# Kernel optimization log

Hardware: AMD Instinct MI355X
Metric: run time of the kernel (lower is better)

## Reference

```python
import jax, jax.numpy as jnp
import numpy as np

N = 100000; E = 1000000; D = 192; FD = 64; L = 6; MLP = 192
TW = 768; NPD = 6; CPD = 7; TEMP = 0.5; NREL = 2; EPS = 1e-5


def _ln(x, g, b):
    mu = jnp.mean(x, axis=-1, keepdims=True)
    var = jnp.mean(jnp.square(x - mu), axis=-1, keepdims=True)
    return (x - mu) * jax.lax.rsqrt(var + EPS) * g + b


def _bn(x, g, b):
    # BatchNorm1d in training mode: batch statistics over the N (node) axis
    mu = jnp.mean(x, axis=0, keepdims=True)
    var = jnp.mean(jnp.square(x - mu), axis=0, keepdims=True)
    return (x - mu) * jax.lax.rsqrt(var + EPS) * g + b


def _rgcn(x, Wrel, Wroot, bias, src, dst, etype):
    # PyG RGCNConv, aggr='mean': out_i = x_i @ Wroot + b + sum_r mean_{j in N_r(i)} x_j @ W_r
    out = x @ Wroot + bias
    for r in range(NREL):
        h = x @ Wrel[r]                                   # [N, D] per-relation transform
        mask = (etype == r)
        msg = jnp.where(mask[:, None], jnp.take(h, src, axis=0), 0.0)  # [E, D]
        agg = jax.ops.segment_sum(msg, dst, num_segments=N)
        cnt = jax.ops.segment_sum(mask.astype(x.dtype), dst, num_segments=N)
        out = out + agg / jnp.maximum(cnt, 1.0)[:, None]
    return out


def _forward(tweet, num_prop, comments_prop,
             Wt, bt, Wn, bnum, Wc, bc,
             Wv, bv, Wo, bo, ln1_g, ln1_b, bn_g, bn_b,
             W1, b1, W2, b2, ln2_g, ln2_b,
             Wrel, Wroot, rgcn_b, Wm1, bm1, Wm2, bm2, Wm3, bm3,
             edge_index, edge_type, labels, train_idx):
    lrelu = jax.nn.leaky_relu  # negative_slope=0.01, same as torch LeakyReLU default
    t = lrelu(tweet @ Wt + bt)
    n = lrelu(num_prop @ Wn + bnum)
    c = lrelu(comments_prop @ Wc + bc)
    x = jnp.concatenate([t, n, c], axis=1)  # [N, D]; seq dim of size 1 is elided
    for i in range(L):
        # MHA over seq_len=1: softmax over a single key is exactly 1, so
        # attn_out = out_proj(v_proj(x)); Q/K projections have zero effect/grad.
        v = x @ Wv[i] + bv[i]
        x = x + (v @ Wo[i] + bo[i])          # dropout in eval mode = identity
        x = _ln(x, ln1_g[i], ln1_b[i])
        x = _bn(x, bn_g[i], bn_b[i])
        f = lrelu(x @ W1[i] + b1[i]) @ W2[i] + b2[i]
        x = x + f
        x = _ln(x, ln2_g[i], ln2_b[i])
    # supervised contrastive loss on first train_idx nodes (train_idx static int)
    feat = x[:train_idx]
    lab = labels[:train_idx]
    fn = feat / jnp.linalg.norm(feat, axis=-1, keepdims=True)
    sim = (fn @ fn.T) / TEMP                              # [T, T]
    ex = jnp.exp(sim)
    match = (lab[:, None] == lab[None, :]).astype(x.dtype)
    closs = jnp.mean(-jnp.log(jnp.sum(match * ex, axis=1) / jnp.sum(ex, axis=1)))
    # two passes through the SAME (shared-weight) RGCN; dropout(p=0.1) eval = identity
    src, dst = edge_index[0], edge_index[1]
    h = _rgcn(x, Wrel, Wroot, rgcn_b, src, dst, edge_type)
    h = _rgcn(h, Wrel, Wroot, rgcn_b, src, dst, edge_type)
    h = lrelu(h @ Wm1 + bm1)
    h = lrelu(h @ Wm2 + bm2)
    logits = h @ Wm3 + bm3                                # [N, 2]
    return logits, closs


def setup_inputs() -> dict:
    key = jax.random.key(0)
    ks = iter(jax.random.split(key, 64))
    f32 = jnp.float32
    def p(*shape):
        fan_in = shape[-2] if len(shape) >= 2 else shape[-1]
        return jax.random.normal(next(ks), shape, f32) * (1.0 / np.sqrt(fan_in))
    inp = {
        'tweet': jax.random.normal(next(ks), (N, TW), f32),
        'num_prop': jax.random.normal(next(ks), (N, NPD), f32),
        'comments_prop': jax.random.normal(next(ks), (N, CPD), f32),
        'Wt': p(TW, FD), 'bt': jnp.zeros((FD,), f32),
        'Wn': p(NPD, FD), 'bnum': jnp.zeros((FD,), f32),
        'Wc': p(CPD, FD), 'bc': jnp.zeros((FD,), f32),
        'Wv': p(L, D, D), 'bv': jnp.zeros((L, D), f32),
        'Wo': p(L, D, D), 'bo': jnp.zeros((L, D), f32),
        'ln1_g': jnp.ones((L, D), f32), 'ln1_b': jnp.zeros((L, D), f32),
        'bn_g': jnp.ones((L, D), f32), 'bn_b': jnp.zeros((L, D), f32),
        'W1': p(L, D, MLP), 'b1': jnp.zeros((L, MLP), f32),
        'W2': p(L, MLP, D), 'b2': jnp.zeros((L, D), f32),
        'ln2_g': jnp.ones((L, D), f32), 'ln2_b': jnp.zeros((L, D), f32),
        'Wrel': p(NREL, D, D), 'Wroot': p(D, D), 'rgcn_b': jnp.zeros((D,), f32),
        'Wm1': p(D, MLP), 'bm1': jnp.zeros((MLP,), f32),
        'Wm2': p(MLP, D), 'bm2': jnp.zeros((D,), f32),
        'Wm3': p(D, 2), 'bm3': jnp.zeros((2,), f32),
        'edge_index': jax.random.randint(next(ks), (2, E), 0, N, jnp.int32),
        'edge_type': jax.random.randint(next(ks), (E,), 0, NREL, jnp.int32),
        'labels': jax.random.randint(next(ks), (N,), 0, 2, jnp.int32),
        'train_idx': 8192,
    }
    return inp


def reference(tweet, num_prop, comments_prop, Wt, bt, Wn, bnum, Wc, bc,
              Wv, bv, Wo, bo, ln1_g, ln1_b, bn_g, bn_b,
              W1, b1, W2, b2, ln2_g, ln2_b,
              Wrel, Wroot, rgcn_b, Wm1, bm1, Wm2, bm2, Wm3, bm3,
              edge_index, edge_type, labels, train_idx):
    return _forward(tweet, num_prop, comments_prop, Wt, bt, Wn, bnum, Wc, bc,
                    Wv, bv, Wo, bo, ln1_g, ln1_b, bn_g, bn_b,
                    W1, b1, W2, b2, ln2_g, ln2_b,
                    Wrel, Wroot, rgcn_b, Wm1, bm1, Wm2, bm2, Wm3, bm3,
                    edge_index, edge_type, labels, train_idx)
```

## Files before the change

kernel.cpp:

```cpp
#include <hip/hip_runtime.h>

#define NN 100000
#define EE 1000000
#define DDIM 192
#define NLAYER 6
#define TRAIN 8192
#define SLOPE 0.01f
#define EPS_LN 1e-5f
#define TOTSEG (2 * NN)
#define SCAN_NB 98

typedef float f32x4 __attribute__((ext_vector_type(4)));
typedef __bf16 bf16x8 __attribute__((ext_vector_type(8)));
typedef unsigned short ushort_t;
typedef unsigned int uint_t;

__device__ __forceinline__ float lrelu(float v) { return v > 0.0f ? v : SLOPE * v; }

__device__ __forceinline__ ushort_t f2bf(float f) {
    __bf16 h = (__bf16)f;
    return __builtin_bit_cast(ushort_t, h);
}

__device__ __forceinline__ float bf2f(ushort_t b) {
    union { uint_t u; float f; } v; v.u = ((uint_t)b) << 16; return v.f;
}

__device__ __forceinline__ float wave_sum(float s) {
    #pragma unroll
    for (int off = 32; off > 0; off >>= 1) s += __shfl_down(s, off);
    return __shfl(s, 0);
}

__global__ __launch_bounds__(256) void prep_w(
    const float* __restrict__ Wt, const float* __restrict__ Wv,
    const float* __restrict__ Wo, const float* __restrict__ W1,
    const float* __restrict__ W2, const float* __restrict__ Wrel,
    const float* __restrict__ Wroot, const float* __restrict__ Wm1,
    const float* __restrict__ Wm2, ushort_t* __restrict__ WTt,
    ushort_t* __restrict__ WTs, ushort_t* __restrict__ WTg)
{
    const int bid = blockIdx.x;
    if (bid < 29 * 144) {
        const int mat = bid / 144;
        const int o = (bid % 144) * 256 + threadIdx.x;
        const float* src;
        if      (mat <  6) src = Wv   + (size_t)mat * 36864;
        else if (mat < 12) src = Wo   + (size_t)(mat - 6)  * 36864;
        else if (mat < 18) src = W1   + (size_t)(mat - 12) * 36864;
        else if (mat < 24) src = W2   + (size_t)(mat - 18) * 36864;
        else if (mat < 26) src = Wrel + (size_t)(mat - 24) * 36864;
        else if (mat == 26) src = Wroot;
        else if (mat == 27) src = Wm1;
        else                src = Wm2;
        const int m = o / 192, k = o - m * 192;
        const ushort_t b = f2bf(src[(size_t)k * 192 + m]);
        if (mat == 24 || mat == 25)
            WTg[(size_t)m * 576 + 192 + (mat - 24) * 192 + k] = b;
        else if (mat == 26)
            WTg[(size_t)m * 576 + k] = b;
        else
            WTs[(size_t)mat * 36864 + o] = b;
    } else {
        const int o = (bid - 29 * 144) * 256 + threadIdx.x;
        const int m = o / 768, k = o - m * 768;
        WTt[o] = f2bf(Wt[(size_t)k * 64 + m]);
    }
}

__global__ __launch_bounds__(512) void gemm_tweet(
    const float* __restrict__ A, const ushort_t* __restrict__ WT,
    const float* __restrict__ bias, ushort_t* __restrict__ Cbf, int n)
{
    __shared__ ushort_t Ws[2][64 * 32];
    const int tid = threadIdx.x;
    const int lane = tid & 63, w = tid >> 6;
    const int quad = lane >> 4, l15 = lane & 15;
    const int row0 = blockIdx.x * 128;
    const int myrow = row0 + w * 16 + l15;
    const bool rok = myrow < n;

    f32x4 acc[4];
    #pragma unroll
    for (int nf = 0; nf < 4; ++nf) acc[nf] = (f32x4){0.f, 0.f, 0.f, 0.f};

    const float* aF = A + (size_t)myrow * 768 + quad * 8;

    auto stageW = [&](int t, int b) {
        if (tid < 256) {
            const int col = tid >> 2, part = tid & 3;
            *(uint4*)&Ws[b][col * 32 + part * 8] =
                *(const uint4*)(WT + (size_t)col * 768 + (t << 5) + part * 8);
        }
    };
    auto loadA = [&](int t, float* fo) {
        if (rok) {
            const float4 p0 = *(const float4*)(aF + t * 32);
            const float4 p1 = *(const float4*)(aF + t * 32 + 4);
            fo[0] = p0.x; fo[1] = p0.y; fo[2] = p0.z; fo[3] = p0.w;
            fo[4] = p1.x; fo[5] = p1.y; fo[6] = p1.z; fo[7] = p1.w;
        } else {
            #pragma unroll
            for (int i = 0; i < 8; ++i) fo[i] = 0.f;
        }
    };

    float fc[8];
    stageW(0, 0);
    loadA(0, fc);
    __syncthreads();
    #pragma unroll 2
    for (int t = 0; t < 24; ++t) {
        const int b = t & 1;
        if (t < 23) stageW(t + 1, b ^ 1);
        float fn[8];
        if (t < 23) loadA(t + 1, fn);
        union { uint_t u[4]; bf16x8 v; } r;
        #pragma unroll
        for (int i = 0; i < 4; ++i)
            r.u[i] = (uint_t)f2bf(fc[2 * i]) | ((uint_t)f2bf(fc[2 * i + 1]) << 16);
        #pragma unroll
        for (int nf = 0; nf < 4; ++nf) {
            const bf16x8 bb = *(const bf16x8*)&Ws[b][(nf * 16 + l15) * 32 + quad * 8];
            acc[nf] = __builtin_amdgcn_mfma_f32_16x16x32_bf16(r.v, bb, acc[nf], 0, 0, 0);
        }
        __syncthreads();
        if (t < 23) {
            #pragma unroll
            for (int i = 0; i < 8; ++i) fc[i] = fn[i];
        }
    }

    #pragma unroll
    for (int reg = 0; reg < 4; ++reg) {
        const int gr = row0 + w * 16 + quad * 4 + reg;
        if (gr >= n) continue;
        #pragma unroll
        for (int nf = 0; nf < 4; ++nf) {
            const int col = nf * 16 + l15;
            Cbf[(size_t)gr * DDIM + col] = f2bf(lrelu(acc[nf][reg] + bias[col]));
        }
    }
}

template <bool RELU1, bool RELU2, bool RES, bool LNORM, bool BN,
          bool BNSTAT, bool CBF, bool LOGITS, bool FNORM>
__global__ __launch_bounds__(512, 4) void gemm2_mfma(
    const ushort_t* __restrict__ Ain, const ushort_t* __restrict__ wta,
    const float* __restrict__ bias1, const ushort_t* __restrict__ wtb,
    const float* __restrict__ bias2, const ushort_t* __restrict__ resin,
    ushort_t* __restrict__ Cbf,
    const float* __restrict__ bnsum, const float* __restrict__ bng,
    const float* __restrict__ bnb, float* __restrict__ bnacc,
    const float* __restrict__ lg, const float* __restrict__ lb,
    const float* __restrict__ Wm3, const float* __restrict__ bm3,
    float* __restrict__ outp, ushort_t* __restrict__ fnb, int n)
{
    constexpr int VST = 200;
    __shared__ ushort_t Vs[128 * VST];
    __shared__ ushort_t Ws[2][192 * 32];
    __shared__ float scs[DDIM], shs[DDIM];
    const int tid = threadIdx.x;
    const int lane = tid & 63, w = tid >> 6;
    const int quad = lane >> 4, l15 = lane & 15;
    const int row0 = blockIdx.x * 128;
    const int myrow = row0 + w * 16 + l15;
    const bool rok = myrow < n;

    if constexpr (BN) {
        const float invN = 1.0f / (float)NN;
        for (int j = tid; j < DDIM; j += 512) {
            const float mu = bnsum[j] * invN;
            const float var = bnsum[DDIM + j] * invN - mu * mu;
            const float sc = bng[j] * rsqrtf(var + EPS_LN);
            scs[j] = sc;
            shs[j] = fmaf(-mu, sc, bnb[j]);
        }
    }

    f32x4 acc[12];
    #pragma unroll
    for (int nf = 0; nf < 12; ++nf) acc[nf] = (f32x4){0.f, 0.f, 0.f, 0.f};

    const ushort_t* aB = Ain + (size_t)myrow * DDIM + quad * 8;

    auto stageW = [&](const ushort_t* wt, int t, int b) {
        const int k0 = t << 5;
        for (int s = tid; s < 768; s += 512) {
            const int col = s >> 2, part = s & 3;
            *(uint4*)&Ws[b][col * 32 + part * 8] =
                *(const uint4*)(wt + (size_t)col * DDIM + k0 + part * 8);
        }
    };
    auto loadA = [&](int t) -> uint4 {
        return rok ? *(const uint4*)(aB + t * 32) : make_uint4(0u, 0u, 0u, 0u);
    };
    auto makeA = [&](const uint4& ui, int t) -> bf16x8 {
        if constexpr (BN) {
            const int c0 = (t << 5) + quad * 8;
            const float4 sc0 = *(const float4*)&scs[c0];
            const float4 sc1 = *(const float4*)&scs[c0 + 4];
            const float4 sh0 = *(const float4*)&shs[c0];
            const float4 sh1 = *(const float4*)&shs[c0 + 4];
            const uint_t* uw = (const uint_t*)&ui;
            float x[8];
            #pragma unroll
            for (int i = 0; i < 4; ++i) {
                x[2 * i]     = bf2f((ushort_t)(uw[i] & 0xffffu));
                x[2 * i + 1] = bf2f((ushort_t)(uw[i] >> 16));
            }
            x[0] = fmaf(x[0], sc0.x, sh0.x); x[1] = fmaf(x[1], sc0.y, sh0.y);
            x[2] = fmaf(x[2], sc0.z, sh0.z); x[3] = fmaf(x[3], sc0.w, sh0.w);
            x[4] = fmaf(x[4], sc1.x, sh1.x); x[5] = fmaf(x[5], sc1.y, sh1.y);
            x[6] = fmaf(x[6], sc1.z, sh1.z); x[7] = fmaf(x[7], sc1.w, sh1.w);
            union { uint_t u[4]; bf16x8 v; } r;
            #pragma unroll
            for (int i = 0; i < 4; ++i)
                r.u[i] = (uint_t)f2bf(x[2 * i]) | ((uint_t)f2bf(x[2 * i + 1]) << 16);
            return r.v;
        } else {
            return __builtin_bit_cast(bf16x8, ui);
        }
    };

    uint4 uc;
    stageW(wta, 0, 0);
    uc = loadA(0);
    __syncthreads();
    #pragma unroll 2
    for (int t = 0; t < 6; ++t) {
        const int b = t & 1;
        if (t < 5) stageW(wta, t + 1, b ^ 1);
        uint4 un;
        if (t < 5) un = loadA(t + 1);
        const bf16x8 a = makeA(uc, t);
        #pragma unroll
        for (int nf = 0; nf < 12; ++nf) {
            const bf16x8 bb = *(const bf16x8*)&Ws[b][(nf * 16 + l15) * 32 + quad * 8];
            acc[nf] = __builtin_amdgcn_mfma_f32_16x16x32_bf16(a, bb, acc[nf], 0, 0, 0);
        }
        __syncthreads();
        if (t < 5) uc = un;
    }

    {
        float b1r[12];
        #pragma unroll
        for (int nf = 0; nf < 12; ++nf) b1r[nf] = bias1[nf * 16 + l15];
        #pragma unroll
        for (int reg = 0; reg < 4; ++reg) {
            ushort_t* vrow = &Vs[(w * 16 + quad * 4 + reg) * VST + l15];
            #pragma unroll
            for (int nf = 0; nf < 12; ++nf) {
                float x = acc[nf][reg] + b1r[nf];
                if (RELU1) x = lrelu(x);
                vrow[nf * 16] = f2bf(x);
                acc[nf][reg] = 0.f;
            }
        }
    }
    stageW(wtb, 0, 0);
    __syncthreads();

    #pragma unroll 2
    for (int t = 0; t < 6; ++t) {
        const int b = t & 1;
        if (t < 5) stageW(wtb, t + 1, b ^ 1);
        const bf16x8 a = *(const bf16x8*)&Vs[(w * 16 + l15) * VST + (t << 5) + quad * 8];
        #pragma unroll
        for (int nf = 0; nf < 12; ++nf) {
            const bf16x8 bb = *(const bf16x8*)&Ws[b][(nf * 16 + l15) * 32 + quad * 8];
            acc[nf] = __builtin_amdgcn_mfma_f32_16x16x32_bf16(a, bb, acc[nf], 0, 0, 0);
        }
        __syncthreads();
    }

    int   col[12];
    float bia[12];
    #pragma unroll
    for (int nf = 0; nf < 12; ++nf) {
        col[nf] = nf * 16 + l15;
        bia[nf] = bias2[col[nf]];
    }
    float rsc[12], rsh[12];
    if constexpr (BN && RES) {
        #pragma unroll
        for (int nf = 0; nf < 12; ++nf) {
            rsc[nf] = scs[col[nf]];
            rsh[nf] = shs[col[nf]];
        }
    }
    float w3a[12], w3b[12];
    if constexpr (LOGITS) {
        #pragma unroll
        for (int nf = 0; nf < 12; ++nf) {
            w3a[nf] = Wm3[col[nf] * 2 + 0];
            w3b[nf] = Wm3[col[nf] * 2 + 1];
        }
    }
    float cs[12], cs2[12];
    if constexpr (BNSTAT) {
        #pragma unroll
        for (int nf = 0; nf < 12; ++nf) { cs[nf] = 0.f; cs2[nf] = 0.f; }
    }
    #pragma unroll
    for (int reg = 0; reg < 4; ++reg) {
        const int gr = row0 + w * 16 + quad * 4 + reg;
        const bool ok = gr < n;
        float v[12];
        #pragma unroll
        for (int nf = 0; nf < 12; ++nf) {
            float x = acc[nf][reg] + bia[nf];
            if constexpr (RES) {
                float r = ok ? bf2f(resin[(size_t)gr * DDIM + col[nf]]) : 0.f;
                if constexpr (BN) r = fmaf(r, rsc[nf], rsh[nf]);
                x += r;
            }
            v[nf] = x;
        }
        if constexpr (LNORM) {
            float s = 0.f, s2 = 0.f;
            #pragma unroll
            for (int nf = 0; nf < 12; ++nf) { s += v[nf]; s2 = fmaf(v[nf], v[nf], s2); }
            #pragma unroll
            for (int off = 1; off < 16; off <<= 1) {
                s  += __shfl_xor(s, off);
                s2 += __shfl_xor(s2, off);
            }
            const float mu = s * (1.0f / DDIM);
            const float var = s2 * (1.0f / DDIM) - mu * mu;
            const float rs = rsqrtf(var + EPS_LN);
            #pragma unroll
            for (int nf = 0; nf < 12; ++nf)
                v[nf] = fmaf((v[nf] - mu) * rs, lg[col[nf]], lb[col[nf]]);
        }
        float s0 = 0.f, s1 = 0.f;
        #pragma unroll
        for (int nf = 0; nf < 12; ++nf) {
            float x = v[nf];
            if (RELU2) x = lrelu(x);
            if constexpr (BNSTAT) {
                const float xa = ok ? x : 0.f;
                cs[nf] += xa;
                cs2[nf] = fmaf(xa, xa, cs2[nf]);
            }
            if constexpr (LOGITS) {
                s0 = fmaf(x, w3a[nf], s0);
                s1 = fmaf(x, w3b[nf], s1);
            }
            if (ok) {
                if constexpr (CBF) Cbf[(size_t)gr * DDIM + col[nf]] = f2bf(x);
            }
        }
        if constexpr (LOGITS) {
            #pragma unroll
            for (int off = 1; off < 16; off <<= 1) {
                s0 += __shfl_xor(s0, off);
                s1 += __shfl_xor(s1, off);
            }
            if (l15 == 0 && ok) {
                outp[(size_t)gr * 2 + 0] = s0 + bm3[0];
                outp[(size_t)gr * 2 + 1] = s1 + bm3[1];
            }
        }
        if constexpr (FNORM) {
            if (gr < TRAIN) {
                float q = 0.f;
                #pragma unroll
                for (int nf = 0; nf < 12; ++nf) q = fmaf(v[nf], v[nf], q);
                #pragma unroll
                for (int off = 1; off < 16; off <<= 1) q += __shfl_xor(q, off);
                const float inv = 1.0f / sqrtf(q);
                #pragma unroll
                for (int nf = 0; nf < 12; ++nf)
                    fnb[(size_t)gr * DDIM + col[nf]] = f2bf(v[nf] * inv);
            }
        }
    }
    if constexpr (BNSTAT) {
        float* bsA = (float*)&Ws[0][0];
        float* bsB = bsA + 8 * 192;
        #pragma unroll
        for (int nf = 0; nf < 12; ++nf) {
            cs[nf]  += __shfl_xor(cs[nf], 16);  cs[nf]  += __shfl_xor(cs[nf], 32);
            cs2[nf] += __shfl_xor(cs2[nf], 16); cs2[nf] += __shfl_xor(cs2[nf], 32);
        }
        if (quad == 0) {
            #pragma unroll
            for (int nf = 0; nf < 12; ++nf) {
                bsA[w * 192 + col[nf]] = cs[nf];
                bsB[w * 192 + col[nf]] = cs2[nf];
            }
        }
        __syncthreads();
        if (tid < DDIM) {
            float s = 0.f, s2 = 0.f;
            #pragma unroll
            for (int k = 0; k < 8; ++k) {
                s  += bsA[k * 192 + tid];
                s2 += bsB[k * 192 + tid];
            }
            atomicAdd(&bnacc[tid], s);
            atomicAdd(&bnacc[DDIM + tid], s2);
        }
    }
}

__global__ __launch_bounds__(512, 4) void gemm_cat(
    const ushort_t* __restrict__ A1, const ushort_t* __restrict__ A2,
    const ushort_t* __restrict__ WT, const float* __restrict__ bias,
    ushort_t* __restrict__ Cbf, int n)
{
    __shared__ ushort_t Ws[2][192 * 32];
    const int tid = threadIdx.x;
    const int lane = tid & 63, w = tid >> 6;
    const int quad = lane >> 4, l15 = lane & 15;
    const int row0 = blockIdx.x * 128;
    const int myrow = row0 + w * 16 + l15;
    const bool rok = myrow < n;

    f32x4 acc[12];
    #pragma unroll
    for (int nf = 0; nf < 12; ++nf) acc[nf] = (f32x4){0.f, 0.f, 0.f, 0.f};

    const ushort_t* a1p = A1 + (size_t)myrow * 192 + quad * 8;
    const ushort_t* a2p = A2 + (size_t)myrow * 384 + quad * 8;

    auto stageW = [&](int t, int b) {
        const int k0 = t << 5;
        for (int s = tid; s < 768; s += 512) {
            const int col = s >> 2, part = s & 3;
            *(uint4*)&Ws[b][col * 32 + part * 8] =
                *(const uint4*)(WT + (size_t)col * 576 + k0 + part * 8);
        }
    };
    auto loadA = [&](int t) -> uint4 {
        if (!rok) return make_uint4(0u, 0u, 0u, 0u);
        const ushort_t* p = (t < 6) ? (a1p + t * 32) : (a2p + (t - 6) * 32);
        return *(const uint4*)p;
    };

    uint4 uc;
    stageW(0, 0);
    uc = loadA(0);
    __syncthreads();

    #pragma unroll 2
    for (int t = 0; t < 18; ++t) {
        const int b = t & 1;
        if (t < 17) stageW(t + 1, b ^ 1);
        uint4 un;
        if (t < 17) un = loadA(t + 1);
        const bf16x8 a = __builtin_bit_cast(bf16x8, uc);
        #pragma unroll
        for (int nf = 0; nf < 12; ++nf) {
            const bf16x8 bb = *(const bf16x8*)&Ws[b][(nf * 16 + l15) * 32 + quad * 8];
            acc[nf] = __builtin_amdgcn_mfma_f32_16x16x32_bf16(a, bb, acc[nf], 0, 0, 0);
        }
        __syncthreads();
        if (t < 17) uc = un;
    }

    #pragma unroll
    for (int reg = 0; reg < 4; ++reg) {
        const int gr = row0 + w * 16 + quad * 4 + reg;
        if (gr >= n) continue;
        #pragma unroll
        for (int nf = 0; nf < 12; ++nf) {
            const int col = nf * 16 + l15;
            Cbf[(size_t)gr * DDIM + col] = f2bf(acc[nf][reg] + bias[col]);
        }
    }
}

__global__ __launch_bounds__(256) void embed_nc_k(
    const float* __restrict__ np_, const float* __restrict__ cp,
    const float* __restrict__ Wn, const float* __restrict__ bnum,
    const float* __restrict__ Wc, const float* __restrict__ bc,
    ushort_t* __restrict__ xb)
{
    const int idx = blockIdx.x * 256 + threadIdx.x;
    if (idx >= NN * 128) return;
    const int node = idx >> 7;
    const int c = idx & 127;
    float acc;
    if (c < 64) {
        acc = bnum[c];
        #pragma unroll
        for (int k = 0; k < 6; ++k) acc = fmaf(np_[node * 6 + k], Wn[k * 64 + c], acc);
    } else {
        const int cc = c - 64;
        acc = bc[cc];
        #pragma unroll
        for (int k = 0; k < 7; ++k) acc = fmaf(cp[node * 7 + k], Wc[k * 64 + cc], acc);
    }
    xb[(size_t)node * DDIM + 64 + c] = f2bf(lrelu(acc));
}

__global__ __launch_bounds__(256) void sim_mfma(const ushort_t* __restrict__ fnb,
    const int* __restrict__ lab, float* __restrict__ row_ex, float* __restrict__ row_mt)
{
    __shared__ ushort_t Ai[128 * 32];
    __shared__ ushort_t Bj[128 * 32];
    __shared__ int Li[128], Lj[128];
    const int bid = blockIdx.x;
    int ti = (int)((sqrtf(8.0f * (float)bid + 1.0f) - 1.0f) * 0.5f);
    while ((ti + 1) * (ti + 2) / 2 <= bid) ++ti;
    while (ti * (ti + 1) / 2 > bid) --ti;
    const int tj = bid - ti * (ti + 1) / 2;
    const int i0 = ti * 128, j0 = tj * 128;
    const bool offd = (ti != tj);

    const int tid = threadIdx.x, lane = tid & 63, w = tid >> 6;
    const int quad = lane >> 4, l15 = lane & 15;
    if (tid < 128) Li[tid] = lab[i0 + tid];
    else           Lj[tid - 128] = lab[j0 + tid - 128];
    const int iw = (w >> 1) * 64, jw = (w & 1) * 64;

    f32x4 acc[4][4];
    #pragma unroll
    for (int m = 0; m < 4; ++m)
        #pragma unroll
        for (int nf = 0; nf < 4; ++nf)
            acc[m][nf] = (f32x4){0.f, 0.f, 0.f, 0.f};

    for (int k0 = 0; k0 < DDIM; k0 += 32) {
        #pragma unroll
        for (int s = tid; s < 512; s += 256) {
            const int row = s >> 2, part = s & 3;
            *(uint4*)&Ai[row * 32 + part * 8] =
                *(const uint4*)(fnb + (size_t)(i0 + row) * DDIM + k0 + part * 8);
            *(uint4*)&Bj[row * 32 + part * 8] =
                *(const uint4*)(fnb + (size_t)(j0 + row) * DDIM + k0 + part * 8);
        }
        __syncthreads();
        bf16x8 a[4], b[4];
        #pragma unroll
        for (int m = 0; m < 4; ++m)
            a[m] = *(const bf16x8*)&Ai[(iw + m * 16 + l15) * 32 + quad * 8];
        #pragma unroll
        for (int nf = 0; nf < 4; ++nf)
            b[nf] = *(const bf16x8*)&Bj[(jw + nf * 16 + l15) * 32 + quad * 8];
        #pragma unroll
        for (int m = 0; m < 4; ++m)
            #pragma unroll
            for (int nf = 0; nf < 4; ++nf)
                acc[m][nf] = __builtin_amdgcn_mfma_f32_16x16x32_bf16(a[m], b[nf], acc[m][nf], 0, 0, 0);
        __syncthreads();
    }

    int lj[4];
    #pragma unroll
    for (int nf = 0; nf < 4; ++nf) lj[nf] = Lj[jw + nf * 16 + l15];
    float ce[4], cm[4];
    #pragma unroll
    for (int nf = 0; nf < 4; ++nf) { ce[nf] = 0.f; cm[nf] = 0.f; }

    #pragma unroll
    for (int m = 0; m < 4; ++m) {
        #pragma unroll
        for (int reg = 0; reg < 4; ++reg) {
            const int rl = iw + m * 16 + quad * 4 + reg;
            const int li = Li[rl];
            float se = 0.f, sm = 0.f;
            #pragma unroll
            for (int nf = 0; nf < 4; ++nf) {
                const float e = __expf(acc[m][nf][reg] * 2.0f);
                se += e;
                const bool mt = (li == lj[nf]);
                if (mt) sm += e;
                if (offd) {
                    ce[nf] += e;
                    if (mt) cm[nf] += e;
                }
            }
            #pragma unroll
            for (int off = 1; off < 16; off <<= 1) {
                se += __shfl_xor(se, off);
                sm += __shfl_xor(sm, off);
            }
            if (l15 == 0) {
                atomicAdd(&row_ex[i0 + rl], se);
                atomicAdd(&row_mt[i0 + rl], sm);
            }
        }
    }
    if (offd) {
        #pragma unroll
        for (int nf = 0; nf < 4; ++nf) {
            ce[nf] += __shfl_xor(ce[nf], 16); ce[nf] += __shfl_xor(ce[nf], 32);
            cm[nf] += __shfl_xor(cm[nf], 16); cm[nf] += __shfl_xor(cm[nf], 32);
        }
        if (quad == 0) {
            #pragma unroll
            for (int nf = 0; nf < 4; ++nf) {
                atomicAdd(&row_ex[j0 + jw + nf * 16 + l15], ce[nf]);
                atomicAdd(&row_mt[j0 + jw + nf * 16 + l15], cm[nf]);
            }
        }
    }
}

__global__ __launch_bounds__(256) void closs_k(const float* __restrict__ ex,
    const float* __restrict__ mt, float* __restrict__ out)
{
    float s = 0.f;
    for (int i = threadIdx.x; i < TRAIN; i += 256) s += -logf(mt[i] / ex[i]);
    s = wave_sum(s);
    __shared__ float red[4];
    const int wave = threadIdx.x >> 6, lane = threadIdx.x & 63;
    if (lane == 0) red[wave] = s;
    __syncthreads();
    if (threadIdx.x == 0) out[0] = (red[0] + red[1] + red[2] + red[3]) / (float)TRAIN;
}

__global__ __launch_bounds__(256) void cnt_i_k(const int* __restrict__ dst,
    const int* __restrict__ ety, int* __restrict__ cnti)
{
    const int e = blockIdx.x * 256 + threadIdx.x;
    if (e >= EE) return;
    atomicAdd(&cnti[(size_t)ety[e] * NN + dst[e]], 1);
}

__global__ __launch_bounds__(256) void part_k(const int* __restrict__ cnti,
                                              int* __restrict__ part)
{
    __shared__ int sh[256];
    const int tid = threadIdx.x;
    const int i0 = blockIdx.x * 2048 + tid * 8;
    int s = 0;
    #pragma unroll
    for (int j = 0; j < 8; ++j) {
        const int i = i0 + j;
        s += (i < TOTSEG) ? cnti[i] : 0;
    }
    sh[tid] = s;
    __syncthreads();
    #pragma unroll
    for (int off = 128; off > 0; off >>= 1) {
        if (tid < off) sh[tid] += sh[tid + off];
        __syncthreads();
    }
    if (tid == 0) part[blockIdx.x] = sh[0];
}

__global__ __launch_bounds__(128) void scanp_k(int* __restrict__ part)
{
    __shared__ int sh[128];
    const int tid = threadIdx.x;
    const int v = (tid < SCAN_NB) ? part[tid] : 0;
    sh[tid] = v;
    __syncthreads();
    #pragma unroll
    for (int off = 1; off < 128; off <<= 1) {
        const int t = (tid >= off) ? sh[tid - off] : 0;
        __syncthreads();
        sh[tid] += t;
        __syncthreads();
    }
    if (tid < SCAN_NB) part[tid] = sh[tid] - v;
}

__global__ __launch_bounds__(256) void offs_k(const int* __restrict__ cnti,
    const int* __restrict__ part, int* __restrict__ offs)
{
    __shared__ int sh[256];
    const int tid = threadIdx.x;
    const int i0 = blockIdx.x * 2048 + tid * 8;
    int v[8];
    int loc = 0;
    #pragma unroll
    for (int j = 0; j < 8; ++j) {
        const int i = i0 + j;
        v[j] = (i < TOTSEG) ? cnti[i] : 0;
        loc += v[j];
    }
    sh[tid] = loc;
    __syncthreads();
    #pragma unroll
    for (int off = 1; off < 256; off <<= 1) {
        const int t = (tid >= off) ? sh[tid - off] : 0;
        __syncthreads();
        sh[tid] += t;
        __syncthreads();
    }
    int pre = part[blockIdx.x] + sh[tid] - loc;
    #pragma unroll
    for (int j = 0; j < 8; ++j) {
        const int i = i0 + j;
        if (i < TOTSEG) offs[i] = pre;
        pre += v[j];
    }
}

__global__ __launch_bounds__(256) void fill_k(const int* __restrict__ src,
    const int* __restrict__ dst, const int* __restrict__ ety,
    int* __restrict__ offs, int* __restrict__ elist)
{
    const int e = blockIdx.x * 256 + threadIdx.x;
    if (e >= EE) return;
    const int pos = atomicAdd(&offs[(size_t)ety[e] * NN + dst[e]], 1);
    elist[pos] = src[e];
}

__global__ __launch_bounds__(256) void gather_bf_k(const ushort_t* __restrict__ xb,
    const int* __restrict__ elist, const int* __restrict__ offs,
    const int* __restrict__ cnti, ushort_t* __restrict__ aggb)
{
    const int wave = threadIdx.x >> 6, lane = threadIdx.x & 63;
    const int d = blockIdx.x * 4 + wave;
    if (d >= NN) return;
    const bool lo = lane < 32;
    #pragma unroll
    for (int r = 0; r < 2; ++r) {
        const int seg = r * NN + d;
        const int end = offs[seg];
        const int c = cnti[seg];
        float a0 = 0.f, a1 = 0.f, b0 = 0.f, b1 = 0.f;
        int e = end - c;
        for (; e + 1 < end; e += 2) {
            const int s0 = elist[e], s1 = elist[e + 1];
            const uint_t* r0 = (const uint_t*)(xb + (size_t)s0 * DDIM);
            const uint_t* r1 = (const uint_t*)(xb + (size_t)s1 * DDIM);
            const uint_t x0 = r0[lane], x1 = r1[lane];
            uint_t y0 = 0u, y1 = 0u;
            if (lo) { y0 = r0[64 + lane]; y1 = r1[64 + lane]; }
            a0 += bf2f((ushort_t)(x0 & 0xffffu)) + bf2f((ushort_t)(x1 & 0xffffu));
            a1 += bf2f((ushort_t)(x0 >> 16))     + bf2f((ushort_t)(x1 >> 16));
            b0 += bf2f((ushort_t)(y0 & 0xffffu)) + bf2f((ushort_t)(y1 & 0xffffu));
            b1 += bf2f((ushort_t)(y0 >> 16))     + bf2f((ushort_t)(y1 >> 16));
        }
        if (e < end) {
            const int s0 = elist[e];
            const uint_t* r0 = (const uint_t*)(xb + (size_t)s0 * DDIM);
            const uint_t x0 = r0[lane];
            uint_t y0 = 0u;
            if (lo) y0 = r0[64 + lane];
            a0 += bf2f((ushort_t)(x0 & 0xffffu));
            a1 += bf2f((ushort_t)(x0 >> 16));
            b0 += bf2f((ushort_t)(y0 & 0xffffu));
            b1 += bf2f((ushort_t)(y0 >> 16));
        }
        const float inv = 1.0f / (float)max(c, 1);
        uint_t* ar = (uint_t*)(aggb + (size_t)d * 384 + r * DDIM);
        ar[lane] = (uint_t)f2bf(a0 * inv) | ((uint_t)f2bf(a1 * inv) << 16);
        if (lo)
            ar[64 + lane] = (uint_t)f2bf(b0 * inv) | ((uint_t)f2bf(b1 * inv) << 16);
    }
}

extern "C" void kernel_launch(void* const* d_in, const int* in_sizes, int n_in,
                              void* d_out, int out_size, void* d_ws, size_t ws_size,
                              hipStream_t stream)
{
    const float* tweet   = (const float*)d_in[0];
    const float* np_     = (const float*)d_in[1];
    const float* cp      = (const float*)d_in[2];
    const float* Wt      = (const float*)d_in[3];
    const float* bt      = (const float*)d_in[4];
    const float* Wn      = (const float*)d_in[5];
    const float* bnum    = (const float*)d_in[6];
    const float* Wc      = (const float*)d_in[7];
    const float* bc      = (const float*)d_in[8];
    const float* Wv      = (const float*)d_in[9];
    const float* bv      = (const float*)d_in[10];
    const float* Wo      = (const float*)d_in[11];
    const float* bo      = (const float*)d_in[12];
    const float* ln1g    = (const float*)d_in[13];
    const float* ln1b    = (const float*)d_in[14];
    const float* bng     = (const float*)d_in[15];
    const float* bnb     = (const float*)d_in[16];
    const float* W1      = (const float*)d_in[17];
    const float* b1      = (const float*)d_in[18];
    const float* W2      = (const float*)d_in[19];
    const float* b2      = (const float*)d_in[20];
    const float* ln2g    = (const float*)d_in[21];
    const float* ln2b    = (const float*)d_in[22];
    const float* Wrel    = (const float*)d_in[23];
    const float* Wroot   = (const float*)d_in[24];
    const float* rgcnb   = (const float*)d_in[25];
    const float* Wm1     = (const float*)d_in[26];
    const float* bm1     = (const float*)d_in[27];
    const float* Wm2     = (const float*)d_in[28];
    const float* bm2     = (const float*)d_in[29];
    const float* Wm3     = (const float*)d_in[30];
    const float* bm3     = (const float*)d_in[31];
    const int*   eidx    = (const int*)d_in[32];
    const int*   esrc    = eidx;
    const int*   edst    = eidx + EE;
    const int*   ety     = (const int*)d_in[33];
    const int*   labels  = (const int*)d_in[34];
    float* out = (float*)d_out;

    const size_t ND = (size_t)NN * DDIM;
    ushort_t* XBF  = (ushort_t*)d_ws;
    ushort_t* X1BF = XBF + ND;
    ushort_t* AGGB = X1BF + ND;
    ushort_t* FNb  = AGGB + 2 * ND;
    ushort_t* WTt  = FNb + (size_t)TRAIN * DDIM;
    ushort_t* WTs  = WTt + 49152;
    ushort_t* WTg  = WTs + (size_t)29 * 36864;
    float* ROWEX = (float*)(WTg + 110592);
    float* ROWMT = ROWEX + TRAIN;
    float* BNS   = ROWMT + TRAIN;
    int*   CNTI  = (int*)(BNS + 12 * DDIM);
    int*   OFFS  = CNTI + 2 * NN;
    int*   ELIST = OFFS + 2 * NN;
    int*   PART  = ELIST + EE;
    ushort_t* WTv  = WTs;
    ushort_t* WTo  = WTs + (size_t)6  * 36864;
    ushort_t* WT1  = WTs + (size_t)12 * 36864;
    ushort_t* WT2  = WTs + (size_t)18 * 36864;
    ushort_t* WTm1 = WTs + (size_t)27 * 36864;
    ushort_t* WTm2 = WTs + (size_t)28 * 36864;

    const int gx = (NN + 127) / 128;
    const dim3 blk(256);
    const dim3 blk5(512);

    prep_w<<<29 * 144 + 192, blk, 0, stream>>>(Wt, Wv, Wo, W1, W2, Wrel, Wroot, Wm1, Wm2, WTt, WTs, WTg);

    hipMemsetAsync(CNTI, 0, 2 * NN * sizeof(int), stream);
    cnt_i_k<<<(EE + 255) / 256, blk, 0, stream>>>(edst, ety, CNTI);
    part_k<<<SCAN_NB, blk, 0, stream>>>(CNTI, PART);
    scanp_k<<<1, 128, 0, stream>>>(PART);
    offs_k<<<SCAN_NB, blk, 0, stream>>>(CNTI, PART, OFFS);
    fill_k<<<(EE + 255) / 256, blk, 0, stream>>>(esrc, edst, ety, OFFS, ELIST);

    gemm_tweet<<<gx, blk5, 0, stream>>>(tweet, WTt, bt, XBF, NN);
    embed_nc_k<<<(NN * 128 + 255) / 256, blk, 0, stream>>>(np_, cp, Wn, bnum, Wc, bc, XBF);

    hipMemsetAsync(BNS, 0, 12 * DDIM * sizeof(float), stream);
    for (int i = 0; i < NLAYER; ++i) {
        const size_t wo = (size_t)i * 36864;
        float* bnacc_i = BNS + (size_t)i * 2 * DDIM;
        gemm2_mfma<false, false, true, true, false, true, true, false, false>
            <<<gx, blk5, 0, stream>>>(
            XBF, WTv + wo, bv + i * DDIM, WTo + wo, bo + i * DDIM, XBF,
            X1BF, nullptr, nullptr, nullptr, bnacc_i,
            ln1g + i * DDIM, ln1b + i * DDIM, nullptr, nullptr, nullptr, nullptr, NN);
        if (i < NLAYER - 1)
            gemm2_mfma<true, false, true, true, true, false, true, false, false>
                <<<gx, blk5, 0, stream>>>(
                X1BF, WT1 + wo, b1 + i * DDIM, WT2 + wo, b2 + i * DDIM, X1BF,
                XBF, bnacc_i, bng + i * DDIM, bnb + i * DDIM, nullptr,
                ln2g + i * DDIM, ln2b + i * DDIM, nullptr, nullptr, nullptr, nullptr, NN);
        else
            gemm2_mfma<true, false, true, true, true, false, true, false, true>
                <<<gx, blk5, 0, stream>>>(
                X1BF, WT1 + wo, b1 + i * DDIM, WT2 + wo, b2 + i * DDIM, X1BF,
                XBF, bnacc_i, bng + i * DDIM, bnb + i * DDIM, nullptr,
                ln2g + i * DDIM, ln2b + i * DDIM, nullptr, nullptr, nullptr, FNb, NN);
    }

    hipMemsetAsync(ROWEX, 0, 2 * TRAIN * sizeof(float), stream);
    sim_mfma<<<(TRAIN / 128) * (TRAIN / 128 + 1) / 2, blk, 0, stream>>>(FNb, labels, ROWEX, ROWMT);
    closs_k<<<1, blk, 0, stream>>>(ROWEX, ROWMT, out + 2 * (size_t)NN);

    gather_bf_k<<<(NN + 3) / 4, blk, 0, stream>>>(XBF, ELIST, OFFS, CNTI, AGGB);
    gemm_cat<<<gx, blk5, 0, stream>>>(XBF, AGGB, WTg, rgcnb, XBF, NN);

    gather_bf_k<<<(NN + 3) / 4, blk, 0, stream>>>(XBF, ELIST, OFFS, CNTI, AGGB);
    gemm_cat<<<gx, blk5, 0, stream>>>(XBF, AGGB, WTg, rgcnb, XBF, NN);

    gemm2_mfma<true, true, false, false, false, false, false, true, false>
        <<<gx, blk5, 0, stream>>>(
        XBF, WTm1, bm1, WTm2, bm2, nullptr, nullptr,
        nullptr, nullptr, nullptr, nullptr, nullptr, nullptr,
        Wm3, bm3, out, nullptr, NN);
}
```

Before: 1.852 ms.

## Stage GEMM epilogue outputs through LDS, fuse embeddings, split gather per relation

```diff
diff --git a/kernel.cpp b/kernel.cpp
--- a/kernel.cpp
+++ b/kernel.cpp
@@ -70,9 +70,15 @@
 
 __global__ __launch_bounds__(512) void gemm_tweet(
     const float* __restrict__ A, const ushort_t* __restrict__ WT,
-    const float* __restrict__ bias, ushort_t* __restrict__ Cbf, int n)
-{
+    const float* __restrict__ bias,
+    const float* __restrict__ np_, const float* __restrict__ cp,
+    const float* __restrict__ Wn, const float* __restrict__ bnum,
+    const float* __restrict__ Wc, const float* __restrict__ bc,
+    ushort_t* __restrict__ Cbf, int n)
+{
+    constexpr int VST = 200;
     __shared__ ushort_t Ws[2][64 * 32];
+    __shared__ ushort_t Cs[128 * VST];
     const int tid = threadIdx.x;
     const int lane = tid & 63, w = tid >> 6;
     const int quad = lane >> 4, l15 = lane & 15;
@@ -133,13 +139,38 @@
 
     #pragma unroll
     for (int reg = 0; reg < 4; ++reg) {
-        const int gr = row0 + w * 16 + quad * 4 + reg;
-        if (gr >= n) continue;
+        const int lrow = w * 16 + quad * 4 + reg;
+        const int gr = row0 + lrow;
         #pragma unroll
         for (int nf = 0; nf < 4; ++nf) {
             const int col = nf * 16 + l15;
-            Cbf[(size_t)gr * DDIM + col] = f2bf(lrelu(acc[nf][reg] + bias[col]));
-        }
+            Cs[lrow * VST + col] = f2bf(lrelu(acc[nf][reg] + bias[col]));
+        }
+        if (gr < n) {
+            const float* nrow = np_ + (size_t)gr * 6;
+            const float* crow = cp + (size_t)gr * 7;
+            for (int cj = 64 + l15; cj < 192; cj += 16) {
+                float a;
+                if (cj < 128) {
+                    const int c = cj - 64;
+                    a = bnum[c];
+                    #pragma unroll
+                    for (int k = 0; k < 6; ++k) a = fmaf(nrow[k], Wn[k * 64 + c], a);
+                } else {
+                    const int cc = cj - 128;
+                    a = bc[cc];
+                    #pragma unroll
+                    for (int k = 0; k < 7; ++k) a = fmaf(crow[k], Wc[k * 64 + cc], a);
+                }
+                Cs[lrow * VST + cj] = f2bf(lrelu(a));
+            }
+        }
+    }
+    if (rok) {
+        const uint4* vp = (const uint4*)&Cs[(size_t)(w * 16 + l15) * VST];
+        uint4* gp = (uint4*)(Cbf + (size_t)myrow * DDIM);
+        #pragma unroll
+        for (int j = 0; j < 6; ++j) gp[quad * 6 + j] = vp[quad * 6 + j];
     }
 }
 
@@ -275,6 +306,15 @@
         __syncthreads();
     }
 
+    if constexpr (RES) {
+        if (rok) {
+            const uint4* rp = (const uint4*)(resin + (size_t)myrow * DDIM);
+            uint4* vp = (uint4*)&Vs[(size_t)(w * 16 + l15) * VST];
+            #pragma unroll
+            for (int j = 0; j < 6; ++j) vp[quad * 6 + j] = rp[quad * 6 + j];
+        }
+    }
+
     int   col[12];
     float bia[12];
     #pragma unroll
@@ -305,14 +345,15 @@
     }
     #pragma unroll
     for (int reg = 0; reg < 4; ++reg) {
-        const int gr = row0 + w * 16 + quad * 4 + reg;
+        const int lrow = w * 16 + quad * 4 + reg;
+        const int gr = row0 + lrow;
         const bool ok = gr < n;
         float v[12];
         #pragma unroll
         for (int nf = 0; nf < 12; ++nf) {
             float x = acc[nf][reg] + bia[nf];
             if constexpr (RES) {
-                float r = ok ? bf2f(resin[(size_t)gr * DDIM + col[nf]]) : 0.f;
+                float r = ok ? bf2f(Vs[lrow * VST + col[nf]]) : 0.f;
                 if constexpr (BN) r = fmaf(r, rsc[nf], rsh[nf]);
                 x += r;
             }
@@ -348,9 +389,7 @@
                 s0 = fmaf(x, w3a[nf], s0);
                 s1 = fmaf(x, w3b[nf], s1);
             }
-            if (ok) {
-                if constexpr (CBF) Cbf[(size_t)gr * DDIM + col[nf]] = f2bf(x);
-            }
+            if constexpr (CBF) Vs[lrow * VST + col[nf]] = f2bf(x);
         }
         if constexpr (LOGITS) {
             #pragma unroll
@@ -377,6 +416,14 @@
             }
         }
     }
+    if constexpr (CBF) {
+        if (rok) {
+            const uint4* vp = (const uint4*)&Vs[(size_t)(w * 16 + l15) * VST];
+            uint4* gp = (uint4*)(Cbf + (size_t)myrow * DDIM);
+            #pragma unroll
+            for (int j = 0; j < 6; ++j) gp[quad * 6 + j] = vp[quad * 6 + j];
+        }
+    }
     if constexpr (BNSTAT) {
         float* bsA = (float*)&Ws[0][0];
         float* bsB = bsA + 8 * 192;
@@ -411,7 +458,9 @@
     const ushort_t* __restrict__ WT, const float* __restrict__ bias,
     ushort_t* __restrict__ Cbf, int n)
 {
+    constexpr int VST = 200;
     __shared__ ushort_t Ws[2][192 * 32];
+    __shared__ ushort_t Cs[128 * VST];
     const int tid = threadIdx.x;
     const int lane = tid & 63, w = tid >> 6;
     const int quad = lane >> 4, l15 = lane & 15;
@@ -463,38 +512,19 @@
 
     #pragma unroll
     for (int reg = 0; reg < 4; ++reg) {
-        const int gr = row0 + w * 16 + quad * 4 + reg;
-        if (gr >= n) continue;
+        const int lrow = w * 16 + quad * 4 + reg;
         #pragma unroll
         for (int nf = 0; nf < 12; ++nf) {
             const int col = nf * 16 + l15;
-            Cbf[(size_t)gr * DDIM + col] = f2bf(acc[nf][reg] + bias[col]);
-        }
-    }
-}
-
-__global__ __launch_bounds__(256) void embed_nc_k(
-    const float* __restrict__ np_, const float* __restrict__ cp,
-    const float* __restrict__ Wn, const float* __restrict__ bnum,
-    const float* __restrict__ Wc, const float* __restrict__ bc,
-    ushort_t* __restrict__ xb)
-{
-    const int idx = blockIdx.x * 256 + threadIdx.x;
-    if (idx >= NN * 128) return;
-    const int node = idx >> 7;
-    const int c = idx & 127;
-    float acc;
-    if (c < 64) {
-        acc = bnum[c];
-        #pragma unroll
-        for (int k = 0; k < 6; ++k) acc = fmaf(np_[node * 6 + k], Wn[k * 64 + c], acc);
-    } else {
-        const int cc = c - 64;
-        acc = bc[cc];
-        #pragma unroll
-        for (int k = 0; k < 7; ++k) acc = fmaf(cp[node * 7 + k], Wc[k * 64 + cc], acc);
-    }
-    xb[(size_t)node * DDIM + 64 + c] = f2bf(lrelu(acc));
+            Cs[lrow * VST + col] = f2bf(acc[nf][reg] + bias[col]);
+        }
+    }
+    if (rok) {
+        const uint4* vp = (const uint4*)&Cs[(size_t)(w * 16 + l15) * VST];
+        uint4* gp = (uint4*)(Cbf + (size_t)myrow * DDIM);
+        #pragma unroll
+        for (int j = 0; j < 6; ++j) gp[quad * 6 + j] = vp[quad * 6 + j];
+    }
 }
 
 __global__ __launch_bounds__(256) void sim_mfma(const ushort_t* __restrict__ fnb,
@@ -708,45 +738,44 @@
     const int* __restrict__ cnti, ushort_t* __restrict__ aggb)
 {
     const int wave = threadIdx.x >> 6, lane = threadIdx.x & 63;
-    const int d = blockIdx.x * 4 + wave;
-    if (d >= NN) return;
+    const int seg = blockIdx.x * 4 + wave;
+    if (seg >= TOTSEG) return;
+    const int r = (seg < NN) ? 0 : 1;
+    const int d = seg - r * NN;
     const bool lo = lane < 32;
-    #pragma unroll
-    for (int r = 0; r < 2; ++r) {
-        const int seg = r * NN + d;
-        const int end = offs[seg];
-        const int c = cnti[seg];
-        float a0 = 0.f, a1 = 0.f, b0 = 0.f, b1 = 0.f;
-        int e = end - c;
-        for (; e + 1 < end; e += 2) {
-            const int s0 = elist[e], s1 = elist[e + 1];
-            const uint_t* r0 = (const uint_t*)(xb + (size_t)s0 * DDIM);
-            const uint_t* r1 = (const uint_t*)(xb + (size_t)s1 * DDIM);
-            const uint_t x0 = r0[lane], x1 = r1[lane];
-            uint_t y0 = 0u, y1 = 0u;
-            if (lo) { y0 = r0[64 + lane]; y1 = r1[64 + lane]; }
-            a0 += bf2f((ushort_t)(x0 & 0xffffu)) + bf2f((ushort_t)(x1 & 0xffffu));
-            a1 += bf2f((ushort_t)(x0 >> 16))     + bf2f((ushort_t)(x1 >> 16));
-            b0 += bf2f((ushort_t)(y0 & 0xffffu)) + bf2f((ushort_t)(y1 & 0xffffu));
-            b1 += bf2f((ushort_t)(y0 >> 16))     + bf2f((ushort_t)(y1 >> 16));
-        }
-        if (e < end) {
-            const int s0 = elist[e];
-            const uint_t* r0 = (const uint_t*)(xb + (size_t)s0 * DDIM);
-            const uint_t x0 = r0[lane];
-            uint_t y0 = 0u;
-            if (lo) y0 = r0[64 + lane];
-            a0 += bf2f((ushort_t)(x0 & 0xffffu));
-            a1 += bf2f((ushort_t)(x0 >> 16));
-            b0 += bf2f((ushort_t)(y0 & 0xffffu));
-            b1 += bf2f((ushort_t)(y0 >> 16));
-        }
-        const float inv = 1.0f / (float)max(c, 1);
-        uint_t* ar = (uint_t*)(aggb + (size_t)d * 384 + r * DDIM);
-        ar[lane] = (uint_t)f2bf(a0 * inv) | ((uint_t)f2bf(a1 * inv) << 16);
-        if (lo)
-            ar[64 + lane] = (uint_t)f2bf(b0 * inv) | ((uint_t)f2bf(b1 * inv) << 16);
-    }
+
+    const int end = offs[seg];
+    const int c = cnti[seg];
+    float a0 = 0.f, a1 = 0.f, b0 = 0.f, b1 = 0.f;
+    int e = end - c;
+    for (; e + 1 < end; e += 2) {
+        const int s0 = elist[e], s1 = elist[e + 1];
+        const uint_t* r0 = (const uint_t*)(xb + (size_t)s0 * DDIM);
+        const uint_t* r1 = (const uint_t*)(xb + (size_t)s1 * DDIM);
+        const uint_t x0 = r0[lane], x1 = r1[lane];
+        uint_t y0 = 0u, y1 = 0u;
+        if (lo) { y0 = r0[64 + lane]; y1 = r1[64 + lane]; }
+        a0 += bf2f((ushort_t)(x0 & 0xffffu)) + bf2f((ushort_t)(x1 & 0xffffu));
+        a1 += bf2f((ushort_t)(x0 >> 16))     + bf2f((ushort_t)(x1 >> 16));
+        b0 += bf2f((ushort_t)(y0 & 0xffffu)) + bf2f((ushort_t)(y1 & 0xffffu));
+        b1 += bf2f((ushort_t)(y0 >> 16))     + bf2f((ushort_t)(y1 >> 16));
+    }
+    if (e < end) {
+        const int s0 = elist[e];
+        const uint_t* r0 = (const uint_t*)(xb + (size_t)s0 * DDIM);
+        const uint_t x0 = r0[lane];
+        uint_t y0 = 0u;
+        if (lo) y0 = r0[64 + lane];
+        a0 += bf2f((ushort_t)(x0 & 0xffffu));
+        a1 += bf2f((ushort_t)(x0 >> 16));
+        b0 += bf2f((ushort_t)(y0 & 0xffffu));
+        b1 += bf2f((ushort_t)(y0 >> 16));
+    }
+    const float inv = 1.0f / (float)max(c, 1);
+    uint_t* ar = (uint_t*)(aggb + (size_t)d * 384 + r * DDIM);
+    ar[lane] = (uint_t)f2bf(a0 * inv) | ((uint_t)f2bf(a1 * inv) << 16);
+    if (lo)
+        ar[64 + lane] = (uint_t)f2bf(b0 * inv) | ((uint_t)f2bf(b1 * inv) << 16);
 }
 
 extern "C" void kernel_launch(void* const* d_in, const int* in_sizes, int n_in,
@@ -800,11 +829,11 @@
     ushort_t* WTt  = FNb + (size_t)TRAIN * DDIM;
     ushort_t* WTs  = WTt + 49152;
     ushort_t* WTg  = WTs + (size_t)29 * 36864;
-    float* ROWEX = (float*)(WTg + 110592);
+    int*   CNTI  = (int*)(WTg + 110592);
+    float* ROWEX = (float*)(CNTI + 2 * NN);
     float* ROWMT = ROWEX + TRAIN;
     float* BNS   = ROWMT + TRAIN;
-    int*   CNTI  = (int*)(BNS + 12 * DDIM);
-    int*   OFFS  = CNTI + 2 * NN;
+    int*   OFFS  = (int*)(BNS + 12 * DDIM);
     int*   ELIST = OFFS + 2 * NN;
     int*   PART  = ELIST + EE;
     ushort_t* WTv  = WTs;
@@ -818,19 +847,17 @@
     const dim3 blk(256);
     const dim3 blk5(512);
 
+    hipMemsetAsync(CNTI, 0, (size_t)(2 * NN + 2 * TRAIN + 12 * DDIM) * 4, stream);
     prep_w<<<29 * 144 + 192, blk, 0, stream>>>(Wt, Wv, Wo, W1, W2, Wrel, Wroot, Wm1, Wm2, WTt, WTs, WTg);
 
-    hipMemsetAsync(CNTI, 0, 2 * NN * sizeof(int), stream);
     cnt_i_k<<<(EE + 255) / 256, blk, 0, stream>>>(edst, ety, CNTI);
     part_k<<<SCAN_NB, blk, 0, stream>>>(CNTI, PART);
     scanp_k<<<1, 128, 0, stream>>>(PART);
     offs_k<<<SCAN_NB, blk, 0, stream>>>(CNTI, PART, OFFS);
     fill_k<<<(EE + 255) / 256, blk, 0, stream>>>(esrc, edst, ety, OFFS, ELIST);
 
-    gemm_tweet<<<gx, blk5, 0, stream>>>(tweet, WTt, bt, XBF, NN);
-    embed_nc_k<<<(NN * 128 + 255) / 256, blk, 0, stream>>>(np_, cp, Wn, bnum, Wc, bc, XBF);
-
-    hipMemsetAsync(BNS, 0, 12 * DDIM * sizeof(float), stream);
+    gemm_tweet<<<gx, blk5, 0, stream>>>(tweet, WTt, bt, np_, cp, Wn, bnum, Wc, bc, XBF, NN);
+
     for (int i = 0; i < NLAYER; ++i) {
         const size_t wo = (size_t)i * 36864;
         float* bnacc_i = BNS + (size_t)i * 2 * DDIM;
@@ -853,14 +880,13 @@
                 ln2g + i * DDIM, ln2b + i * DDIM, nullptr, nullptr, nullptr, FNb, NN);
     }
 
-    hipMemsetAsync(ROWEX, 0, 2 * TRAIN * sizeof(float), stream);
     sim_mfma<<<(TRAIN / 128) * (TRAIN / 128 + 1) / 2, blk, 0, stream>>>(FNb, labels, ROWEX, ROWMT);
     closs_k<<<1, blk, 0, stream>>>(ROWEX, ROWMT, out + 2 * (size_t)NN);
 
-    gather_bf_k<<<(NN + 3) / 4, blk, 0, stream>>>(XBF, ELIST, OFFS, CNTI, AGGB);
+    gather_bf_k<<<(TOTSEG + 3) / 4, blk, 0, stream>>>(XBF, ELIST, OFFS, CNTI, AGGB);
     gemm_cat<<<gx, blk5, 0, stream>>>(XBF, AGGB, WTg, rgcnb, XBF, NN);
 
-    gather_bf_k<<<(NN + 3) / 4, blk, 0, stream>>>(XBF, ELIST, OFFS, CNTI, AGGB);
+    gather_bf_k<<<(TOTSEG + 3) / 4, blk, 0, stream>>>(XBF, ELIST, OFFS, CNTI, AGGB);
     gemm_cat<<<gx, blk5, 0, stream>>>(XBF, AGGB, WTg, rgcnb, XBF, NN);
 
     gemm2_mfma<true, true, false, false, false, false, false, true, false>
```

Result: no change. 1.817 ms (-1.9%).
